# Kernel tuning notes

Measured on AMD Instinct MI355X. Metric: run time of the kernel, lower is better.

Reference implementation:

```python
import jax, jax.numpy as jnp
import numpy as np

B, MAX_ATOM, N_FEAT = 64, 128, 128
DENSITY = 0.1  # fraction of nonzero off-diagonal Laplacian entries


def setup_inputs() -> dict:
    key = jax.random.key(0)
    k1, k2, k3, k4 = jax.random.split(key, 4)
    node_features = jax.random.normal(k1, (B, MAX_ATOM, N_FEAT), dtype=jnp.float32)
    u = jax.random.uniform(k2, (B, MAX_ATOM, MAX_ATOM))
    vals = jax.random.normal(k3, (B, MAX_ATOM, MAX_ATOM), dtype=jnp.float32)
    lap = jnp.where(u < DENSITY, vals, 0.0)
    eye = jnp.eye(MAX_ATOM, dtype=jnp.float32)[None]
    laplacian = lap * (1.0 - eye) + eye  # diagonal always nonzero (degree term)
    # per-molecule true atom counts in [1, MAX_ATOM]
    n_atoms = jax.random.randint(k4, (B,), 1, MAX_ATOM + 1, dtype=jnp.int32)
    mol_slice = jnp.stack([n_atoms, jnp.full((B,), N_FEAT, jnp.int32)], axis=1)
    l_slice = jnp.stack([n_atoms, n_atoms], axis=1)
    return {"node_features": node_features, "laplacian": laplacian,
            "mol_slice": mol_slice, "l_slice": l_slice}


def _pool_one(x, L, n):
    # x: [A, F], L: [A, A], n: scalar valid atom count
    A = x.shape[0]
    valid = jnp.arange(A) < n                             # [A]
    mask = (L != 0) & valid[None, :] & valid[:, None]     # [A, A] neighbor mask
    # masked max over neighbors j of x[j]
    neigh = jnp.where(mask[:, :, None], x[None, :, :], -jnp.inf)  # [A, A, F]
    pooled = jnp.max(neigh, axis=1)                       # [A, F]
    has_nb = jnp.any(mask, axis=1)                        # [A]
    pooled = jnp.where(has_nb[:, None], pooled, x)        # fallback to self
    return jnp.where(valid[:, None], pooled, 0.0)         # zero-pad to max_atom


def reference(node_features, laplacian, mol_slice, l_slice):
    n_atoms = mol_slice[:, 0]
    return jax.vmap(_pool_one)(node_features, laplacian, n_atoms)
```

## Files before the change

### kernel.cpp

```cpp
#include <hip/hip_runtime.h>
#include <math.h>


#define MAX_ATOM 128
#define N_FEAT 128

__global__ __launch_bounds__(N_FEAT) void GraphPoolMol_kernel(
    const float* __restrict__ x,
    const float* __restrict__ L,
    const int* __restrict__ mol_slice,
    float* __restrict__ out)
{
    const int i = blockIdx.x;
    const int b = blockIdx.y;
    const int f = threadIdx.x;

    const int n = mol_slice[b * 2];

    const size_t base = ((size_t)b * MAX_ATOM + i) * N_FEAT;
    float* orow = out + base;

    if (i >= n) {
        orow[f] = 0.0f;
        return;
    }

    const float* __restrict__ xb   = x + (size_t)b * MAX_ATOM * N_FEAT;
    const float* __restrict__ Lrow = L + ((size_t)b * MAX_ATOM + i) * MAX_ATOM;

    __shared__ int nbr[MAX_ATOM];
    __shared__ int cnt;
    if (f == 0) cnt = 0;
    __syncthreads();

    float lv = (f < n) ? Lrow[f] : 0.0f;
    if (lv != 0.0f) {
        int pos = atomicAdd(&cnt, 1);
        nbr[pos] = f;
    }
    __syncthreads();

    const int m = cnt;
    float acc = -INFINITY;
    for (int k = 0; k < m; ++k) {
        const int j = nbr[k];
        acc = fmaxf(acc, xb[(size_t)j * N_FEAT + f]);
    }
    if (m == 0) acc = xb[(size_t)i * N_FEAT + f];
    orow[f] = acc;
}

extern "C" void kernel_launch(void* const* d_in, const int* in_sizes, int n_in,
                              void* d_out, int out_size, void* d_ws, size_t ws_size,
                              hipStream_t stream) {
    const float* x   = (const float*)d_in[0];
    const float* L   = (const float*)d_in[1];
    const int* mol   = (const int*)d_in[2];
    float* out = (float*)d_out;

    dim3 grid(MAX_ATOM, 64);
    dim3 block(N_FEAT);
    GraphPoolMol_kernel<<<grid, block, 0, stream>>>(x, L, mol, out);
}
```

Measured before the change: 67.73 us.

## Map one wavefront per atom row with ballot-based neighbor compaction and float2 loads

Each atom row is now handled by a single 64-lane wavefront, with four rows per block. Neighbor lists are compacted using ballot, mbcnt and popcount instead of shared-memory atomics and block barriers. Feature and Laplacian accesses use float2 vector loads, and the gather-max loop is unrolled by four so several row loads are in flight at once. The cost is a reliance on wave-synchronous shared-memory visibility, enforced only by an explicit s_waitcnt with no barrier.

```diff
diff --git a/kernel.cpp b/kernel.cpp
--- a/kernel.cpp
+++ b/kernel.cpp
@@ -4,50 +4,77 @@
 
 #define MAX_ATOM 128
 #define N_FEAT 128
+#define B_SIZE 64
+#define WAVES_PER_BLOCK 4
 
-__global__ __launch_bounds__(N_FEAT) void GraphPoolMol_kernel(
+__global__ __launch_bounds__(64 * WAVES_PER_BLOCK) void GraphPoolMol_kernel(
     const float* __restrict__ x,
     const float* __restrict__ L,
     const int* __restrict__ mol_slice,
     float* __restrict__ out)
 {
-    const int i = blockIdx.x;
-    const int b = blockIdx.y;
-    const int f = threadIdx.x;
+    const int lane = threadIdx.x & 63;
+    const int w    = threadIdx.x >> 6;
+    const int i    = blockIdx.x * WAVES_PER_BLOCK + w;
+    const int b    = blockIdx.y;
 
     const int n = mol_slice[b * 2];
 
-    const size_t base = ((size_t)b * MAX_ATOM + i) * N_FEAT;
-    float* orow = out + base;
+    float2* __restrict__ orow =
+        (float2*)(out + ((size_t)b * MAX_ATOM + i) * N_FEAT);
 
     if (i >= n) {
-        orow[f] = 0.0f;
+        orow[lane] = make_float2(0.0f, 0.0f);
         return;
     }
 
-    const float* __restrict__ xb   = x + (size_t)b * MAX_ATOM * N_FEAT;
-    const float* __restrict__ Lrow = L + ((size_t)b * MAX_ATOM + i) * MAX_ATOM;
+    const float* __restrict__ xb = x + (size_t)b * MAX_ATOM * N_FEAT;
+    const float2* __restrict__ Lrow =
+        (const float2*)(L + ((size_t)b * MAX_ATOM + i) * MAX_ATOM);
 
-    __shared__ int nbr[MAX_ATOM];
-    __shared__ int cnt;
-    if (f == 0) cnt = 0;
-    __syncthreads();
+    __shared__ int nbr[WAVES_PER_BLOCK][MAX_ATOM];
 
-    float lv = (f < n) ? Lrow[f] : 0.0f;
-    if (lv != 0.0f) {
-        int pos = atomicAdd(&cnt, 1);
-        nbr[pos] = f;
+    const float2 lv = Lrow[lane];
+    const int  j0 = 2 * lane, j1 = 2 * lane + 1;
+    const bool p0 = (j0 < n) && (lv.x != 0.0f);
+    const bool p1 = (j1 < n) && (lv.y != 0.0f);
+    const unsigned long long m0 = __ballot(p0);
+    const unsigned long long m1 = __ballot(p1);
+    const int below0 = __builtin_amdgcn_mbcnt_hi((unsigned)(m0 >> 32),
+                        __builtin_amdgcn_mbcnt_lo((unsigned)m0, 0u));
+    const int below1 = __builtin_amdgcn_mbcnt_hi((unsigned)(m1 >> 32),
+                        __builtin_amdgcn_mbcnt_lo((unsigned)m1, 0u));
+    const int c0 = __popcll(m0);
+    const int m  = c0 + __popcll(m1);
+    if (p0) nbr[w][below0]      = j0;
+    if (p1) nbr[w][c0 + below1] = j1;
+    asm volatile("s_waitcnt lgkmcnt(0)" ::: "memory");
+
+    float ax = -INFINITY, ay = -INFINITY;
+    int k = 0;
+    for (; k + 4 <= m; k += 4) {
+        const int ja = nbr[w][k + 0];
+        const int jb = nbr[w][k + 1];
+        const int jc = nbr[w][k + 2];
+        const int jd = nbr[w][k + 3];
+        const float2 va = ((const float2*)(xb + (size_t)ja * N_FEAT))[lane];
+        const float2 vb = ((const float2*)(xb + (size_t)jb * N_FEAT))[lane];
+        const float2 vc = ((const float2*)(xb + (size_t)jc * N_FEAT))[lane];
+        const float2 vd = ((const float2*)(xb + (size_t)jd * N_FEAT))[lane];
+        ax = fmaxf(ax, fmaxf(fmaxf(va.x, vb.x), fmaxf(vc.x, vd.x)));
+        ay = fmaxf(ay, fmaxf(fmaxf(va.y, vb.y), fmaxf(vc.y, vd.y)));
     }
-    __syncthreads();
-
-    const int m = cnt;
-    float acc = -INFINITY;
-    for (int k = 0; k < m; ++k) {
-        const int j = nbr[k];
-        acc = fmaxf(acc, xb[(size_t)j * N_FEAT + f]);
+    for (; k < m; ++k) {
+        const int j = nbr[w][k];
+        const float2 v = ((const float2*)(xb + (size_t)j * N_FEAT))[lane];
+        ax = fmaxf(ax, v.x);
+        ay = fmaxf(ay, v.y);
     }
-    if (m == 0) acc = xb[(size_t)i * N_FEAT + f];
-    orow[f] = acc;
+    if (m == 0) {
+        const float2 v = ((const float2*)(xb + (size_t)i * N_FEAT))[lane];
+        ax = v.x; ay = v.y;
+    }
+    orow[lane] = make_float2(ax, ay);
 }
 
 extern "C" void kernel_launch(void* const* d_in, const int* in_sizes, int n_in,
@@ -58,7 +85,7 @@
     const int* mol   = (const int*)d_in[2];
     float* out = (float*)d_out;
 
-    dim3 grid(MAX_ATOM, 64);
-    dim3 block(N_FEAT);
+    dim3 grid(MAX_ATOM / WAVES_PER_BLOCK, B_SIZE);
+    dim3 block(64 * WAVES_PER_BLOCK);
     GraphPoolMol_kernel<<<grid, block, 0, stream>>>(x, L, mol, out);
 }
```

After: 65.01 us. 4.0% less time.
